# Kernel optimization log

Measured on AMD Instinct MI355X. Metric: run time of the kernel, lower is better.

The kernel has to match this reference:

```python
import jax, jax.numpy as jnp
import numpy as np

C = 66  # channels (joints)
NB_CLASSES = 14
T = 96


def conv1d(x, w, b, pad, groups=1):
    # x: (N, Cin, L), w: (Cout, Cin//groups, K)
    y = jax.lax.conv_general_dilated(
        x, w, window_strides=(1,), padding=[(pad, pad)],
        feature_group_count=groups, dimension_numbers=('NCH', 'OIH', 'NCH'))
    return y + b[None, :, None]


def pool2(x):
    # AvgPool1d(kernel_size=2) along last axis
    return x.reshape(*x.shape[:-1], x.shape[-1] // 2, 2).mean(-1)


def setup_inputs() -> dict:
    key = jax.random.key(0)
    ks = jax.random.split(key, 16)

    def xavier(k, shape, fan_in, fan_out, gain=jnp.sqrt(2.0)):
        bound = gain * jnp.sqrt(6.0 / (fan_in + fan_out))
        return jax.random.uniform(k, shape, jnp.float32, -bound, bound)

    B = 2048
    x = jax.random.normal(ks[0], (B, T, C), jnp.float32)
    # shared convs (same weights for every channel)
    w_hs = xavier(ks[1], (8, 1, 7), 1 * 7, 8 * 7)
    b_hs = jnp.full((8,), 0.1, jnp.float32)
    w_ls = xavier(ks[2], (8, 1, 3), 1 * 3, 8 * 3)
    b_ls = jnp.full((8,), 0.1, jnp.float32)
    # per-channel individual convs, packed for grouped conv (groups=C)
    w_hi1 = xavier(ks[3], (C * 4, 8, 7), 8 * 7, 4 * 7)
    b_hi1 = jnp.full((C * 4,), 0.1, jnp.float32)
    w_hi2 = xavier(ks[4], (C * 4, 4, 7), 4 * 7, 4 * 7)
    b_hi2 = jnp.full((C * 4,), 0.1, jnp.float32)
    w_li1 = xavier(ks[5], (C * 4, 8, 3), 8 * 3, 4 * 3)
    b_li1 = jnp.full((C * 4,), 0.1, jnp.float32)
    w_li2 = xavier(ks[6], (C * 4, 4, 3), 4 * 3, 4 * 3)
    b_li2 = jnp.full((C * 4,), 0.1, jnp.float32)
    # MLP
    F_IN = 9 * C * 12
    w_fc1 = xavier(ks[7], (1936, F_IN), F_IN, 1936)
    b_fc1 = jnp.full((1936,), 0.1, jnp.float32)
    w_fc2 = xavier(ks[8], (NB_CLASSES, 1936), 1936, NB_CLASSES)
    b_fc2 = jnp.full((NB_CLASSES,), 0.1, jnp.float32)
    return dict(x=x, w_hs=w_hs, b_hs=b_hs, w_ls=w_ls, b_ls=b_ls,
                w_hi1=w_hi1, b_hi1=b_hi1, w_hi2=w_hi2, b_hi2=b_hi2,
                w_li1=w_li1, b_li1=b_li1, w_li2=w_li2, b_li2=b_li2,
                w_fc1=w_fc1, b_fc1=b_fc1, w_fc2=w_fc2, b_fc2=b_fc2)


def _branch(xc_flat, B, w_s, b_s, w_i1, b_i1, w_i2, b_i2, pad):
    # xc_flat: (B*C, 1, T). Shared conv applied per channel, then grouped
    # (per-channel) convs with groups=C.
    h = pool2(jax.nn.relu(conv1d(xc_flat, w_s, b_s, pad)))       # (B*C, 8, 48)
    h = h.reshape(B, C * 8, T // 2)
    h = pool2(jax.nn.relu(conv1d(h, w_i1, b_i1, pad, groups=C)))  # (B, C*4, 24)
    h = pool2(jax.nn.relu(conv1d(h, w_i2, b_i2, pad, groups=C)))  # (B, C*4, 12)
    return h.reshape(B, C, 4, T // 8)


def reference(x, w_hs, b_hs, w_ls, b_ls, w_hi1, b_hi1, w_hi2, b_hi2,
              w_li1, b_li1, w_li2, b_li2, w_fc1, b_fc1, w_fc2, b_fc2):
    B = x.shape[0]
    xc = jnp.transpose(x, (0, 2, 1))            # (B, C, T)
    xc_flat = xc.reshape(B * C, 1, T)
    high = _branch(xc_flat, B, w_hs, b_hs, w_hi1, b_hi1, w_hi2, b_hi2, pad=3)
    low = _branch(xc_flat, B, w_ls, b_ls, w_li1, b_li1, w_li2, b_li2, pad=1)
    orig = pool2(pool2(pool2(xc)))[:, :, None, :]  # (B, C, 1, 12)
    # per-channel concat order: [original, low, high] -> (B, C, 9, 12)
    feat = jnp.concatenate([orig, low, high], axis=2).reshape(B, 9 * C * 12)
    h = jax.nn.relu(feat @ w_fc1.T + b_fc1)
    return h @ w_fc2.T + b_fc2
```

## Files before the change

kernel.cpp:

```cpp
#include <hip/hip_runtime.h>
#include <hip/hip_bf16.h>

#define T_LEN 96
#define C_CH  66
#define FIN   7128
#define KPAD  7168
#define NFC1  1936
#define NPAD  2048
#define NCLS  14

typedef __bf16 bf16x8 __attribute__((ext_vector_type(8)));
typedef float  f32x4  __attribute__((ext_vector_type(4)));

#define GLD_LDS(gp, lp) __builtin_amdgcn_global_load_lds(                     \
    (__attribute__((address_space(1))) void*)(gp),                            \
    (__attribute__((address_space(3))) void*)(lp), 16, 0, 0)

__global__ __launch_bounds__(256) void transpose_kernel(
    const float* __restrict__ x, float* __restrict__ xT, int B)
{
    __shared__ float tile[64][65];
    const int t = threadIdx.x & 63;
    const int w = threadIdx.x >> 6;
    const int tc0 = blockIdx.x * 64;
    const int b0  = blockIdx.y * 64;
    #pragma unroll
    for (int j = 0; j < 16; j++) {
        const int r = w * 16 + j;
        tile[r][t] = x[(size_t)(b0 + r) * (T_LEN * C_CH) + tc0 + t];
    }
    __syncthreads();
    #pragma unroll
    for (int j = 0; j < 16; j++) {
        const int r = w * 16 + j;
        xT[(size_t)(tc0 + r) * B + b0 + t] = tile[t][r];
    }
}

__global__ __launch_bounds__(256) void pad_w_kernel(
    const float* __restrict__ w, __hip_bfloat16* __restrict__ wb)
{
    int idx = blockIdx.x * 256 + threadIdx.x;
    int row = idx / 896;
    int cc  = idx - row * 896;
    float4 a = {0.f, 0.f, 0.f, 0.f}, b = {0.f, 0.f, 0.f, 0.f};
    if (row < NFC1 && cc < 891) {
        const float4* src = (const float4*)(w + (size_t)row * FIN + cc * 8);
        a = src[0];
        b = src[1];
    }
    __align__(16) __hip_bfloat16 v[8];
    v[0] = __float2bfloat16(a.x); v[1] = __float2bfloat16(a.y);
    v[2] = __float2bfloat16(a.z); v[3] = __float2bfloat16(a.w);
    v[4] = __float2bfloat16(b.x); v[5] = __float2bfloat16(b.y);
    v[6] = __float2bfloat16(b.z); v[7] = __float2bfloat16(b.w);
    *(int4*)(wb + (size_t)row * KPAD + cc * 8) = *(const int4*)v;
}

template <int K, bool DO_EXTRA>
__device__ __forceinline__ void conv_branch(
    const float* __restrict__ xb, int ts,
    const float* __restrict__ wS, const float* __restrict__ bS,
    const float* __restrict__ wi1, const float* __restrict__ bi1,
    const float* __restrict__ wi2, const float* __restrict__ bi2,
    __hip_bfloat16* __restrict__ frow, int out_off)
{
    constexpr int PAD = K / 2;
    constexpr int XW  = 24 + 6 * PAD;
    constexpr int THW = 12 + 2 * PAD;

    float s2phR[4][24];

    #pragma unroll
    for (int tt = 0; tt < 4; tt++) {
        float xw[XW];
        #pragma unroll
        for (int i = 0; i < XW; i++) {
            const int t = 24 * tt - 3 * PAD + i;
            xw[i] = (t >= 0 && t < T_LEN) ? xb[(size_t)t * ts] : 0.f;
        }

        if (DO_EXTRA) {
            #pragma unroll
            for (int r = 0; r < 3; r++) {
                float s = 0.f;
                #pragma unroll
                for (int k = 0; k < 8; k++) s += xw[3 * PAD + 8 * r + k];
                frow[3 * tt + r] = __float2bfloat16(s * 0.125f);
            }
        }

        float s2a[4][12];
        #pragma unroll
        for (int oc = 0; oc < 4; oc++) {
            const float bv = bi1[oc];
            #pragma unroll
            for (int q = 0; q < 12; q++) s2a[oc][q] = bv;
        }

        #pragma unroll 1
        for (int ic = 0; ic < 8; ic++) {
            const float bs1 = bS[ic];
            float thw[THW];
            #pragma unroll
            for (int j = 0; j < THW; j++) {
                const int jg = 12 * tt - PAD + j;
                if (jg < 0 || jg >= 48) { thw[j] = 0.f; continue; }
                float y0 = bs1, y1 = bs1;
                #pragma unroll
                for (int k = 0; k < K; k++) {
                    const float w = wS[ic * K + k];
                    y0 = fmaf(w, xw[2 * j + k], y0);
                    y1 = fmaf(w, xw[2 * j + 1 + k], y1);
                }
                thw[j] = 0.5f * (fmaxf(y0, 0.f) + fmaxf(y1, 0.f));
            }
            #pragma unroll
            for (int q = 0; q < 12; q++) {
                #pragma unroll
                for (int oc = 0; oc < 4; oc++) {
                    float a = s2a[oc][q];
                    #pragma unroll
                    for (int k = 0; k < K; k++)
                        a = fmaf(wi1[(oc * 8 + ic) * K + k], thw[q + k], a);
                    s2a[oc][q] = a;
                }
            }
        }

        #pragma unroll
        for (int oc = 0; oc < 4; oc++)
            #pragma unroll
            for (int r = 0; r < 6; r++)
                s2phR[oc][6 * tt + r] =
                    0.5f * (fmaxf(s2a[oc][2 * r], 0.f) +
                            fmaxf(s2a[oc][2 * r + 1], 0.f));
    }

    #pragma unroll 1
    for (int oc = 0; oc < 4; oc++) {
        const float bv = bi2[oc];
        #pragma unroll
        for (int q = 0; q < 12; q++) {
            float y0 = bv, y1 = bv;
            #pragma unroll
            for (int ic = 0; ic < 4; ic++) {
                #pragma unroll
                for (int k = 0; k < K; k++) {
                    const float w = wi2[(oc * 4 + ic) * K + k];
                    const int i0 = 2 * q + k - PAD;
                    const int i1 = 2 * q + 1 + k - PAD;
                    if (i0 >= 0 && i0 < 24) y0 = fmaf(w, s2phR[ic][i0], y0);
                    if (i1 >= 0 && i1 < 24) y1 = fmaf(w, s2phR[ic][i1], y1);
                }
            }
            frow[out_off + oc * 12 + q] =
                __float2bfloat16(0.5f * (fmaxf(y0, 0.f) + fmaxf(y1, 0.f)));
        }
    }
}

__global__ __launch_bounds__(64, 2) void conv_fused_kernel(
    const float* __restrict__ x, int ts, int bs, int cs,
    const float* __restrict__ w_hs, const float* __restrict__ b_hs,
    const float* __restrict__ w_ls, const float* __restrict__ b_ls,
    const float* __restrict__ w_hi1, const float* __restrict__ b_hi1,
    const float* __restrict__ w_hi2, const float* __restrict__ b_hi2,
    const float* __restrict__ w_li1, const float* __restrict__ b_li1,
    const float* __restrict__ w_li2, const float* __restrict__ b_li2,
    __hip_bfloat16* __restrict__ feat)
{
    const int lane = threadIdx.x;
    const int b = blockIdx.x * 64 + lane;
    const int c = blockIdx.y;
    const float* xb = x + (size_t)b * bs + (size_t)c * cs;
    __hip_bfloat16* frow = feat + (size_t)b * KPAD + c * 108;

    if (blockIdx.z == 0) {
        conv_branch<7, false>(xb, ts, w_hs, b_hs,
                              w_hi1 + c * 224, b_hi1 + c * 4,
                              w_hi2 + c * 112, b_hi2 + c * 4, frow, 60);
    } else {
        if (c == 0) {
            int4* tail = (int4*)(feat + (size_t)b * KPAD + FIN);
            const int4 z = {0, 0, 0, 0};
            #pragma unroll
            for (int i = 0; i < 5; i++) tail[i] = z;
        }
        conv_branch<3, true>(xb, ts, w_ls, b_ls,
                             w_li1 + c * 96, b_li1 + c * 4,
                             w_li2 + c * 48, b_li2 + c * 4, frow, 12);
    }
}

__global__ __launch_bounds__(512, 2) void gemm_kernel(
    const __hip_bfloat16* __restrict__ A,
    const __hip_bfloat16* __restrict__ Bw,
    float* __restrict__ Cm, int kchunk)
{
    __shared__ __align__(16) __hip_bfloat16 lds[2][2][2][8192];

    const int tid  = threadIdx.x;
    const int lane = tid & 63;
    const int wid  = tid >> 6;
    const int m0 = blockIdx.y * 256;
    const int n0 = blockIdx.x * 256;
    const int wm = (wid >> 2) * 128;
    const int wn = (wid & 3) * 64;
    const int lr = lane & 15;
    const int quad = lane >> 4;

    const int csw  = tid ^ ((tid >> 3) & 7);
    const int srow = csw >> 2, scol = (csw & 3) * 8;
    const __hip_bfloat16* gA = A  + (size_t)(m0 + srow) * KPAD + scol;
    const __hip_bfloat16* gB = Bw + (size_t)(n0 + srow) * KPAD + scol;

    f32x4 acc[8][4] = {};

    const int kBeg = blockIdx.z * kchunk;
    const int numt = kchunk >> 6;

#define STAGE_H(opidx, gptr, kh, kt)                                          \
    do {                                                                      \
        const size_t co = (size_t)(kBeg + (kt) * 64 + (kh) * 32);             \
        GLD_LDS((gptr) + co, &lds[(kt) & 1][opidx][kh][wid * 512]);           \
        GLD_LDS((gptr) + co + (size_t)128 * KPAD,                             \
                &lds[(kt) & 1][opidx][kh][4096 + wid * 512]);                 \
    } while (0)

#define SWZ(r, q) (((r) * 32 + (q) * 8) ^ ((((r) >> 1) & 7) << 3))

    STAGE_H(0, gA, 0, 0);
    STAGE_H(1, gB, 0, 0);
    STAGE_H(0, gA, 1, 0);
    STAGE_H(1, gB, 1, 0);

    for (int t = 0; t < numt; ++t) {
        const int p = t & 1;
        const bool pf = (t + 1 < numt);

        if (pf) asm volatile("s_waitcnt vmcnt(4)" ::: "memory");
        else    asm volatile("s_waitcnt vmcnt(0)" ::: "memory");
        __builtin_amdgcn_sched_barrier(0);
        __builtin_amdgcn_s_barrier();
        __builtin_amdgcn_sched_barrier(0);
        {
            bf16x8 bfr[4], af[4];
            #pragma unroll
            for (int nn = 0; nn < 4; nn++)
                bfr[nn] = *(const bf16x8*)&lds[p][1][0][
                    SWZ(wn + nn * 16 + lr, quad)];
            #pragma unroll
            for (int i = 0; i < 4; i++)
                af[i] = *(const bf16x8*)&lds[p][0][0][
                    SWZ(wm + i * 16 + lr, quad)];
            if (pf) STAGE_H(0, gA, 0, t + 1);
            __builtin_amdgcn_s_setprio(1);
            #pragma unroll
            for (int i = 0; i < 4; i++)
                #pragma unroll
                for (int nn = 0; nn < 4; nn++)
                    acc[i][nn] = __builtin_amdgcn_mfma_f32_16x16x32_bf16(
                        af[i], bfr[nn], acc[i][nn], 0, 0, 0);
            __builtin_amdgcn_s_setprio(0);

            #pragma unroll
            for (int i = 0; i < 4; i++)
                af[i] = *(const bf16x8*)&lds[p][0][0][
                    SWZ(wm + 64 + i * 16 + lr, quad)];
            if (pf) STAGE_H(1, gB, 0, t + 1);
            __builtin_amdgcn_s_setprio(1);
            #pragma unroll
            for (int i = 0; i < 4; i++)
                #pragma unroll
                for (int nn = 0; nn < 4; nn++)
                    acc[4 + i][nn] = __builtin_amdgcn_mfma_f32_16x16x32_bf16(
                        af[i], bfr[nn], acc[4 + i][nn], 0, 0, 0);
            __builtin_amdgcn_s_setprio(0);
        }

        if (pf) asm volatile("s_waitcnt vmcnt(4)" ::: "memory");
        else    asm volatile("s_waitcnt vmcnt(0)" ::: "memory");
        __builtin_amdgcn_sched_barrier(0);
        __builtin_amdgcn_s_barrier();
        __builtin_amdgcn_sched_barrier(0);
        {
            bf16x8 bfr[4], af[4];
            #pragma unroll
            for (int nn = 0; nn < 4; nn++)
                bfr[nn] = *(const bf16x8*)&lds[p][1][1][
                    SWZ(wn + nn * 16 + lr, quad)];
            #pragma unroll
            for (int i = 0; i < 4; i++)
                af[i] = *(const bf16x8*)&lds[p][0][1][
                    SWZ(wm + i * 16 + lr, quad)];
            if (pf) STAGE_H(0, gA, 1, t + 1);
            __builtin_amdgcn_s_setprio(1);
            #pragma unroll
            for (int i = 0; i < 4; i++)
                #pragma unroll
                for (int nn = 0; nn < 4; nn++)
                    acc[i][nn] = __builtin_amdgcn_mfma_f32_16x16x32_bf16(
                        af[i], bfr[nn], acc[i][nn], 0, 0, 0);
            __builtin_amdgcn_s_setprio(0);

            #pragma unroll
            for (int i = 0; i < 4; i++)
                af[i] = *(const bf16x8*)&lds[p][0][1][
                    SWZ(wm + 64 + i * 16 + lr, quad)];
            if (pf) STAGE_H(1, gB, 1, t + 1);
            __builtin_amdgcn_s_setprio(1);
            #pragma unroll
            for (int i = 0; i < 4; i++)
                #pragma unroll
                for (int nn = 0; nn < 4; nn++)
                    acc[4 + i][nn] = __builtin_amdgcn_mfma_f32_16x16x32_bf16(
                        af[i], bfr[nn], acc[4 + i][nn], 0, 0, 0);
            __builtin_amdgcn_s_setprio(0);
        }
    }
#undef SWZ
#undef STAGE_H

    float* Cs = Cm + (size_t)blockIdx.z * NPAD * NPAD;
    #pragma unroll
    for (int mt = 0; mt < 8; mt++) {
        #pragma unroll
        for (int nn = 0; nn < 4; nn++) {
            const int col = n0 + wn + nn * 16 + lr;
            const int rb  = m0 + wm + mt * 16 + quad * 4;
            #pragma unroll
            for (int r = 0; r < 4; r++)
                Cs[(size_t)(rb + r) * NPAD + col] = acc[mt][nn][r];
        }
    }
}

__global__ __launch_bounds__(256) void fc2_kernel(
    const float* __restrict__ h1, const float* __restrict__ b1,
    const float* __restrict__ w2, const float* __restrict__ b2,
    float* __restrict__ out, int nslab)
{
    const int b = blockIdx.x;
    const int tid = threadIdx.x;
    float acc[NCLS];
    #pragma unroll
    for (int o = 0; o < NCLS; o++) acc[o] = 0.f;
    for (int n = tid; n < NFC1; n += 256) {
        float hv = b1[n];
        for (int s = 0; s < nslab; s++)
            hv += h1[(size_t)s * NPAD * NPAD + (size_t)b * NPAD + n];
        float h = fmaxf(hv, 0.f);
        #pragma unroll
        for (int o = 0; o < NCLS; o++)
            acc[o] = fmaf(h, w2[o * NFC1 + n], acc[o]);
    }
    __shared__ float red[4][NCLS];
    #pragma unroll
    for (int o = 0; o < NCLS; o++) {
        float v = acc[o];
        #pragma unroll
        for (int s = 32; s > 0; s >>= 1) v += __shfl_down(v, s);
        if ((tid & 63) == 0) red[tid >> 6][o] = v;
    }
    __syncthreads();
    if (tid < NCLS)
        out[b * NCLS + tid] = red[0][tid] + red[1][tid] + red[2][tid] +
                              red[3][tid] + b2[tid];
}

extern "C" void kernel_launch(void* const* d_in, const int* in_sizes, int n_in,
                              void* d_out, int out_size, void* d_ws, size_t ws_size,
                              hipStream_t stream)
{
    (void)n_in; (void)out_size;
    const float* x     = (const float*)d_in[0];
    const float* w_hs  = (const float*)d_in[1];
    const float* b_hs  = (const float*)d_in[2];
    const float* w_ls  = (const float*)d_in[3];
    const float* b_ls  = (const float*)d_in[4];
    const float* w_hi1 = (const float*)d_in[5];
    const float* b_hi1 = (const float*)d_in[6];
    const float* w_hi2 = (const float*)d_in[7];
    const float* b_hi2 = (const float*)d_in[8];
    const float* w_li1 = (const float*)d_in[9];
    const float* b_li1 = (const float*)d_in[10];
    const float* w_li2 = (const float*)d_in[11];
    const float* b_li2 = (const float*)d_in[12];
    const float* w_fc1 = (const float*)d_in[13];
    const float* b_fc1 = (const float*)d_in[14];
    const float* w_fc2 = (const float*)d_in[15];
    const float* b_fc2 = (const float*)d_in[16];
    float* out = (float*)d_out;

    const int B = in_sizes[0] / (T_LEN * C_CH);

    char* ws = (char*)d_ws;
    const size_t featB = (size_t)B * KPAD * 2;
    const size_t wbB   = (size_t)NPAD * KPAD * 2;
    const size_t slabB = (size_t)NPAD * NPAD * 4;
    const size_t xtB   = (size_t)T_LEN * C_CH * B * 4;
    const size_t base2 = featB + wbB;

    __hip_bfloat16* feat = (__hip_bfloat16*)ws;
    __hip_bfloat16* wb   = (__hip_bfloat16*)(ws + featB);
    float* h1            = (float*)(ws + base2);

    const int sk = (ws_size >= base2 + 4 * slabB) ? 4 : 2;
    const bool use_xt = (ws_size >= base2 + sk * slabB + xtB);
    float* xT = (float*)(ws + base2 + sk * slabB);

    pad_w_kernel<<<dim3((NPAD * 896) / 256), 256, 0, stream>>>(w_fc1, wb);

    const float* cx = x;
    int ts = C_CH, bsi = T_LEN * C_CH, cs = 1;
    if (use_xt) {
        transpose_kernel<<<dim3(99, B / 64), 256, 0, stream>>>(x, xT, B);
        cx = xT; ts = C_CH * B; bsi = 1; cs = B;
    }
    conv_fused_kernel<<<dim3(B / 64, C_CH, 2), 64, 0, stream>>>(
        cx, ts, bsi, cs, w_hs, b_hs, w_ls, b_ls,
        w_hi1, b_hi1, w_hi2, b_hi2, w_li1, b_li1, w_li2, b_li2, feat);
    gemm_kernel<<<dim3(NPAD / 256, B / 256, sk), 512, 0, stream>>>(
        feat, wb, h1, KPAD / sk);
    fc2_kernel<<<dim3(B), 256, 0, stream>>>(h1, b_fc1, w_fc2, b_fc2, out, sk);
}
```

Measured before the change: 404.2 us.

## Merge transpose and weight-pad kernels and swizzle GEMM block order

Combines the input transpose and the fc1 weight bf16 conversion/padding into one prep kernel launch, with block index ranges selecting the role. This removes a launch and lets both memory-bound jobs share the GPU at once. Separately, GEMM blocks are remapped into 2x4 tile groups so that co-scheduled blocks share A and B panels, aiming at better L2 reuse. The swizzle assumes the grid is 8 N-tiles by 8 M-tiles, which holds only for B=2048.

Measured after the change: 399.0 us. No clear change (-1.3%).

```diff
diff --git a/kernel.cpp b/kernel.cpp
--- a/kernel.cpp
+++ b/kernel.cpp
@@ -16,45 +16,47 @@
     (__attribute__((address_space(1))) void*)(gp),                            \
     (__attribute__((address_space(3))) void*)(lp), 16, 0, 0)
 
-__global__ __launch_bounds__(256) void transpose_kernel(
-    const float* __restrict__ x, float* __restrict__ xT, int B)
-{
-    __shared__ float tile[64][65];
-    const int t = threadIdx.x & 63;
-    const int w = threadIdx.x >> 6;
-    const int tc0 = blockIdx.x * 64;
-    const int b0  = blockIdx.y * 64;
-    #pragma unroll
-    for (int j = 0; j < 16; j++) {
-        const int r = w * 16 + j;
-        tile[r][t] = x[(size_t)(b0 + r) * (T_LEN * C_CH) + tc0 + t];
-    }
-    __syncthreads();
-    #pragma unroll
-    for (int j = 0; j < 16; j++) {
-        const int r = w * 16 + j;
-        xT[(size_t)(tc0 + r) * B + b0 + t] = tile[t][r];
-    }
-}
-
-__global__ __launch_bounds__(256) void pad_w_kernel(
+__global__ __launch_bounds__(256) void prep_kernel(
+    const float* __restrict__ x, float* __restrict__ xT, int B,
     const float* __restrict__ w, __hip_bfloat16* __restrict__ wb)
 {
-    int idx = blockIdx.x * 256 + threadIdx.x;
-    int row = idx / 896;
-    int cc  = idx - row * 896;
-    float4 a = {0.f, 0.f, 0.f, 0.f}, b = {0.f, 0.f, 0.f, 0.f};
-    if (row < NFC1 && cc < 891) {
-        const float4* src = (const float4*)(w + (size_t)row * FIN + cc * 8);
-        a = src[0];
-        b = src[1];
-    }
-    __align__(16) __hip_bfloat16 v[8];
-    v[0] = __float2bfloat16(a.x); v[1] = __float2bfloat16(a.y);
-    v[2] = __float2bfloat16(a.z); v[3] = __float2bfloat16(a.w);
-    v[4] = __float2bfloat16(b.x); v[5] = __float2bfloat16(b.y);
-    v[6] = __float2bfloat16(b.z); v[7] = __float2bfloat16(b.w);
-    *(int4*)(wb + (size_t)row * KPAD + cc * 8) = *(const int4*)v;
+    const int nTrans = 99 * (B >> 6);
+    const int blk = blockIdx.x;
+    if (blk < nTrans) {
+        __shared__ float tile[64][65];
+        const int by = blk / 99, bx = blk - by * 99;
+        const int t = threadIdx.x & 63;
+        const int wv = threadIdx.x >> 6;
+        const int tc0 = bx * 64;
+        const int b0  = by * 64;
+        #pragma unroll
+        for (int j = 0; j < 16; j++) {
+            const int r = wv * 16 + j;
+            tile[r][t] = x[(size_t)(b0 + r) * (T_LEN * C_CH) + tc0 + t];
+        }
+        __syncthreads();
+        #pragma unroll
+        for (int j = 0; j < 16; j++) {
+            const int r = wv * 16 + j;
+            xT[(size_t)(tc0 + r) * B + b0 + t] = tile[t][r];
+        }
+    } else {
+        int idx = (blk - nTrans) * 256 + threadIdx.x;
+        int row = idx / 896;
+        int cc  = idx - row * 896;
+        float4 a = {0.f, 0.f, 0.f, 0.f}, b = {0.f, 0.f, 0.f, 0.f};
+        if (row < NFC1 && cc < 891) {
+            const float4* src = (const float4*)(w + (size_t)row * FIN + cc * 8);
+            a = src[0];
+            b = src[1];
+        }
+        __align__(16) __hip_bfloat16 v[8];
+        v[0] = __float2bfloat16(a.x); v[1] = __float2bfloat16(a.y);
+        v[2] = __float2bfloat16(a.z); v[3] = __float2bfloat16(a.w);
+        v[4] = __float2bfloat16(b.x); v[5] = __float2bfloat16(b.y);
+        v[6] = __float2bfloat16(b.z); v[7] = __float2bfloat16(b.w);
+        *(int4*)(wb + (size_t)row * KPAD + cc * 8) = *(const int4*)v;
+    }
 }
 
 template <int K, bool DO_EXTRA>
@@ -203,8 +205,10 @@
     const int tid  = threadIdx.x;
     const int lane = tid & 63;
     const int wid  = tid >> 6;
-    const int m0 = blockIdx.y * 256;
-    const int n0 = blockIdx.x * 256;
+    const int sup = blockIdx.x;
+    const int loc = blockIdx.y;
+    const int m0 = ((sup >> 1) * 2 + (loc >> 2)) * 256;
+    const int n0 = ((sup & 1) * 4 + (loc & 3)) * 256;
     const int wm = (wid >> 2) * 128;
     const int wn = (wid & 3) * 64;
     const int lr = lane & 15;
@@ -410,13 +414,15 @@
     const bool use_xt = (ws_size >= base2 + sk * slabB + xtB);
     float* xT = (float*)(ws + base2 + sk * slabB);
 
-    pad_w_kernel<<<dim3((NPAD * 896) / 256), 256, 0, stream>>>(w_fc1, wb);
-
     const float* cx = x;
     int ts = C_CH, bsi = T_LEN * C_CH, cs = 1;
     if (use_xt) {
-        transpose_kernel<<<dim3(99, B / 64), 256, 0, stream>>>(x, xT, B);
+        prep_kernel<<<dim3(99 * (B / 64) + (NPAD * 896) / 256), 256, 0,
+                      stream>>>(x, xT, B, w_fc1, wb);
         cx = xT; ts = C_CH * B; bsi = 1; cs = B;
+    } else {
+        prep_kernel<<<dim3((NPAD * 896) / 256), 256, 0, stream>>>(
+            x, xT, 0, w_fc1, wb);
     }
     conv_fused_kernel<<<dim3(B / 64, C_CH, 2), 64, 0, stream>>>(
         cx, ts, bsi, cs, w_hs, b_hs, w_ls, b_ls,
```
